# Kernel tuning notes

Measured on AMD Instinct MI355X. Metric: run time of the kernel, lower is better.

Reference implementation:

```python
import jax, jax.numpy as jnp
import numpy as np

EMBED_DIM = 128
N_HEADS = 8
TANH_CLIP = 10.0
NEG_INF = -1e9


def setup_inputs() -> dict:
    key = jax.random.key(0)
    k1, k2, k3, k4 = jax.random.split(key, 4)
    B, N, D = 512, 200, EMBED_DIM
    s = 1.0 / np.sqrt(D)
    return {
        "embeddings": jax.random.normal(k1, (B, N, D), dtype=jnp.float32),
        "W_node": jax.random.uniform(k2, (D, 3 * D), jnp.float32, -s, s),
        "W_fixed": jax.random.uniform(k3, (D, D), jnp.float32, -s, s),
        "W_step": jax.random.uniform(k4, (D, D), jnp.float32, -s, s),
    }


def _decode(embeddings, W_node, W_fixed, W_step):
    B, N, D = embeddings.shape
    H = N_HEADS
    dk = D // H

    # Precompute (once): glimpse K/V and logit K, plus fixed graph context.
    proj = embeddings @ W_node                      # [B,N,3D]
    gK, gV, lK = jnp.split(proj, 3, axis=-1)
    gK = gK.reshape(B, N, H, dk).transpose(0, 2, 1, 3)   # [B,H,N,dk]
    gV = gV.reshape(B, N, H, dk).transpose(0, 2, 1, 3)   # [B,H,N,dk]
    graph_emb = embeddings.mean(axis=1)             # [B,D]
    fixed_ctx = graph_emb @ W_fixed                 # [B,D]

    inv_sqrt_dk = 1.0 / jnp.sqrt(jnp.asarray(dk, embeddings.dtype))
    inv_sqrt_d = 1.0 / jnp.sqrt(jnp.asarray(D, embeddings.dtype))
    batch_idx = jnp.arange(B)

    def step(carry, _):
        visited, ctx_emb = carry                    # [B,N] bool, [B,D]
        q = fixed_ctx + ctx_emb @ W_step            # [B,D]
        qh = q.reshape(B, H, dk)                    # [B,H,dk]
        # glimpse multi-head attention (mask_inner=True)
        compat = jnp.einsum('bhd,bhnd->bhn', qh, gK) * inv_sqrt_dk
        compat = jnp.where(visited[:, None, :], NEG_INF, compat)
        attn = jax.nn.softmax(compat, axis=-1)
        glimpse = jnp.einsum('bhn,bhnd->bhd', attn, gV).reshape(B, D)
        # single-head logits with tanh clipping (mask_logits=True)
        logits = jnp.einsum('bd,bnd->bn', glimpse, lK) * inv_sqrt_d
        logits = TANH_CLIP * jnp.tanh(logits)
        logits = jnp.where(visited, NEG_INF, logits)
        log_p = jax.nn.log_softmax(logits, axis=-1)  # [B,N]
        sel = jnp.argmax(log_p, axis=-1)             # greedy [B]
        visited = visited.at[batch_idx, sel].set(True)
        ctx_emb = embeddings[batch_idx, sel]         # next step context
        return (visited, ctx_emb), (log_p, sel)

    init = (jnp.zeros((B, N), dtype=bool), graph_emb)
    _, (log_ps, sels) = jax.lax.scan(step, init, None, length=N)
    return log_ps.transpose(1, 0, 2), sels.transpose(1, 0)  # [B,T,N], [B,T]


def reference(embeddings, W_node, W_fixed, W_step):
    log_p, pi = _decode(embeddings, W_node, W_fixed, W_step)
    return log_p, pi
```

## Files before the change

### kernel.cpp

```cpp
#include <hip/hip_runtime.h>
#include <math.h>


#define Bsz 512
#define Nn  200
#define Dd  128
#define TANH_CLIP 10.0f
#define NEG_INF  -1e9f
#define LOG2E 1.4426950408889634f
#define LN2   0.6931471805599453f
#define QSCALE (0.25f * LOG2E)
#define LSCALE (0.08838834764831845f * 2.0f * LOG2E)

typedef float v2f __attribute__((ext_vector_type(2)));

__device__ __forceinline__ v2f pkfma(v2f a, v2f b, v2f c) {
    return __builtin_elementwise_fma(a, b, c);
}
__device__ __forceinline__ float fast_rcp(float x) { return __builtin_amdgcn_rcpf(x); }
__device__ __forceinline__ float fexp2(float x)    { return __builtin_amdgcn_exp2f(x); }
__device__ __forceinline__ float flog2(float x)    { return __builtin_amdgcn_logf(x); }
__device__ __forceinline__ float rdlane(float v, int l) {
    union { float f; int i; } u; u.f = v;
    u.i = __builtin_amdgcn_readlane(u.i, l);
    return u.f;
}

template <int CTRL, int RMASK, bool BC>
__device__ __forceinline__ float dppf(float x, float oldv) {
    int r = __builtin_amdgcn_update_dpp(__builtin_bit_cast(int, oldv),
                                        __builtin_bit_cast(int, x),
                                        CTRL, RMASK, 0xf, BC);
    return __builtin_bit_cast(float, r);
}
template <int CTRL, int RMASK, bool BC>
__device__ __forceinline__ int dppi(int x, int oldv) {
    return __builtin_amdgcn_update_dpp(oldv, x, CTRL, RMASK, 0xf, BC);
}
__device__ __forceinline__ float wave_sum63(float x) {
    x += dppf<0x111, 0xf, true >(x, 0.f);
    x += dppf<0x112, 0xf, true >(x, 0.f);
    x += dppf<0x114, 0xf, true >(x, 0.f);
    x += dppf<0x118, 0xf, true >(x, 0.f);
    x += dppf<0x142, 0xa, false>(x, 0.f);
    x += dppf<0x143, 0xc, false>(x, 0.f);
    return x;
}
__device__ __forceinline__ float wave_max63(float x) {
    x = fmaxf(x, dppf<0x111, 0xf, false>(x, -INFINITY));
    x = fmaxf(x, dppf<0x112, 0xf, false>(x, -INFINITY));
    x = fmaxf(x, dppf<0x114, 0xf, false>(x, -INFINITY));
    x = fmaxf(x, dppf<0x118, 0xf, false>(x, -INFINITY));
    x = fmaxf(x, dppf<0x142, 0xa, false>(x, -INFINITY));
    x = fmaxf(x, dppf<0x143, 0xc, false>(x, -INFINITY));
    return x;
}

__device__ __forceinline__ float dot16pk(const float4* g4, const float4* q4) {
    const v2f* g = (const v2f*)g4;
    const v2f* q = (const v2f*)q4;
    v2f a0 = g[0] * q[0];
    v2f a1 = g[1] * q[1];
    a0 = pkfma(g[2], q[2], a0);
    a1 = pkfma(g[3], q[3], a1);
    a0 = pkfma(g[4], q[4], a0);
    a1 = pkfma(g[5], q[5], a1);
    a0 = pkfma(g[6], q[6], a0);
    a1 = pkfma(g[7], q[7], a1);
    const v2f a = a0 + a1;
    return a.x + a.y;
}

__global__ __launch_bounds__(256, 3) void proj_kernel(
    const float* __restrict__ emb, const float* __restrict__ Wn,
    float* __restrict__ gk, float* __restrict__ gv, float* __restrict__ lk)
{
    const int bid = blockIdx.x;
    const int cg  = bid % 3;
    const int rowBase = (bid / 3) * 64;
    const int t  = threadIdx.x;
    const int c4 = t & 31;
    const int r8 = t >> 5;

    __shared__ __align__(16) float wn_s[64][128];
    __shared__ __align__(16) float e_s[64][68];

    float acc[8][4];
#pragma unroll
    for (int j = 0; j < 8; ++j)
#pragma unroll
        for (int m = 0; m < 4; ++m) acc[j][m] = 0.f;

    for (int kh = 0; kh < 2; ++kh) {
#pragma unroll
        for (int i = 0; i < 8; ++i) {
            const int idx = t + 256 * i;
            const int kr = idx >> 5, cc = (idx & 31) * 4;
            *(float4*)&wn_s[kr][cc] =
                *(const float4*)&Wn[(size_t)(kh * 64 + kr) * 384 + 128 * cg + cc];
        }
#pragma unroll
        for (int i = 0; i < 4; ++i) {
            const int idx = t + 256 * i;
            const int rr = idx >> 4, kk4 = (idx & 15) * 4;
            *(float4*)&e_s[rr][kk4] =
                *(const float4*)&emb[(size_t)(rowBase + rr) * Dd + kh * 64 + kk4];
        }
        __syncthreads();

#pragma unroll
        for (int k4 = 0; k4 < 16; ++k4) {
            float4 er[8];
#pragma unroll
            for (int j = 0; j < 8; ++j)
                er[j] = *(const float4*)&e_s[8 * r8 + j][4 * k4];
#pragma unroll
            for (int m = 0; m < 4; ++m) {
                const float4 wv = *(const float4*)&wn_s[4 * k4 + m][4 * c4];
#pragma unroll
                for (int j = 0; j < 8; ++j) {
                    const float ev = (m == 0) ? er[j].x : (m == 1) ? er[j].y
                                   : (m == 2) ? er[j].z : er[j].w;
                    acc[j][0] = fmaf(ev, wv.x, acc[j][0]);
                    acc[j][1] = fmaf(ev, wv.y, acc[j][1]);
                    acc[j][2] = fmaf(ev, wv.z, acc[j][2]);
                    acc[j][3] = fmaf(ev, wv.w, acc[j][3]);
                }
            }
        }
        __syncthreads();
    }

    float* out = (cg == 0) ? gk : (cg == 1) ? gv : lk;
    const float scl = (cg == 0) ? QSCALE : (cg == 2) ? LSCALE : 1.0f;
#pragma unroll
    for (int j = 0; j < 8; ++j) {
        float4 v;
        v.x = acc[j][0] * scl; v.y = acc[j][1] * scl;
        v.z = acc[j][2] * scl; v.w = acc[j][3] * scl;
        *(float4*)&out[(size_t)(rowBase + 8 * r8 + j) * Dd + 4 * c4] = v;
    }
}

__global__ __launch_bounds__(512, 2) void decode_kernel(
    const float* __restrict__ emb,
    const float* __restrict__ Wf,
    const float* __restrict__ Wsp,
    const float* __restrict__ gk, const float* __restrict__ gv,
    const float* __restrict__ lk,
    float* __restrict__ out_logp,
    float* __restrict__ out_pi)
{
    const int b    = blockIdx.x;
    const int t    = threadIdx.x;
    const int lane = t & 63;
    const int w    = t >> 6;
    const int g    = t >> 7;
    const int d    = t & 127;
    const int jq   = lane >> 2;
    const int kk   = lane & 3;

    __shared__ __align__(16) float qall_s[201 * Dd];
    __shared__ __align__(16) float wchunk_s[16][Dd];
    __shared__ __align__(16) float red[4][Dd];
    __shared__ __align__(16) float ctx0_s[Dd];
    __shared__ __align__(16) float fixedc_s[Dd];
    __shared__ __align__(16) float sm2[8][256];
    __shared__ __align__(16) float glimbc[8][16];
    __shared__             float smp[256 * 9];
    __shared__ __align__(16) float4 cand[8];

    const float* embB = emb + (size_t)b * Nn * Dd;
    const float* gkB  = gk  + (size_t)b * Nn * Dd;
    const float* gvB  = gv  + (size_t)b * Nn * Dd;
    const float* lkB  = lk  + (size_t)b * Nn * Dd;

    {
        const float4* e4  = (const float4*)embB;
        float4*       es4 = (float4*)qall_s;
#pragma unroll
        for (int it = 0; it < 12; ++it) es4[t + 512 * it] = e4[t + 512 * it];
        if (t < 256) es4[t + 6144] = e4[t + 6144];
    }
    __syncthreads();
    {
        float s = 0.f;
#pragma unroll
        for (int k = 0; k < 50; ++k) s += qall_s[(50 * g + k) * Dd + d];
        red[g][d] = s;
    }
    __syncthreads();
    if (t < 128) ctx0_s[t] = (red[0][t] + red[1][t] + red[2][t] + red[3][t]) * (1.0f / 200.0f);
    __syncthreads();
    {
        float s = 0.f;
#pragma unroll
        for (int j = 0; j < 32; ++j)
            s = fmaf(ctx0_s[32 * g + j], Wf[(32 * g + j) * Dd + d], s);
        red[g][d] = s;
    }
    __syncthreads();
    if (t < 128) {
        fixedc_s[t] = red[0][t] + red[1][t] + red[2][t] + red[3][t];
        qall_s[200 * Dd + t] = ctx0_s[t];
    }
    __syncthreads();

    float qr[52];
#pragma unroll
    for (int i = 0; i < 52; ++i) qr[i] = 0.f;
    for (int kc = 0; kc < 8; ++kc) {
        {
            const int kr = t >> 5, cc = (t & 31) * 4;
            *(float4*)&wchunk_s[kr][cc] =
                *(const float4*)&Wsp[(size_t)(16 * kc + kr) * Dd + cc];
        }
        __syncthreads();
#pragma unroll
        for (int i = 0; i < 52; ++i) {
            const int r = 52 * g + i;
            if (r < 201) {
#pragma unroll
                for (int j4 = 0; j4 < 4; ++j4) {
                    const float4 ev = *(const float4*)&qall_s[r * Dd + 16 * kc + 4 * j4];
                    qr[i] = fmaf(ev.x, wchunk_s[4 * j4 + 0][d], qr[i]);
                    qr[i] = fmaf(ev.y, wchunk_s[4 * j4 + 1][d], qr[i]);
                    qr[i] = fmaf(ev.z, wchunk_s[4 * j4 + 2][d], qr[i]);
                    qr[i] = fmaf(ev.w, wchunk_s[4 * j4 + 3][d], qr[i]);
                }
            }
        }
        __syncthreads();
    }
#pragma unroll
    for (int i = 0; i < 52; ++i) {
        const int r = 52 * g + i;
        if (r < 201) qall_s[r * Dd + d] = qr[i];
    }
    __syncthreads();

    float4 gk0[4], gk1[4], gk2[4], gk3[4];
    float4 lr[4][4];
    float  gva[52];
    float  cb[4];
    {
        const int n3 = (lane < 8) ? lane + 192 : 199;
        const float4* s0 = (const float4*)(gkB + (size_t)(lane      ) * Dd + 16 * w);
        const float4* s1 = (const float4*)(gkB + (size_t)(lane +  64) * Dd + 16 * w);
        const float4* s2 = (const float4*)(gkB + (size_t)(lane + 128) * Dd + 16 * w);
        const float4* s3 = (const float4*)(gkB + (size_t)n3 * Dd + 16 * w);
#pragma unroll
        for (int i = 0; i < 4; ++i) { gk0[i]=s0[i]; gk1[i]=s1[i]; gk2[i]=s2[i]; gk3[i]=s3[i]; }
        const float4* l0 = (const float4*)(lkB + (size_t)(lane      ) * Dd + 16 * w);
        const float4* l1 = (const float4*)(lkB + (size_t)(lane +  64) * Dd + 16 * w);
        const float4* l2 = (const float4*)(lkB + (size_t)(lane + 128) * Dd + 16 * w);
        const float4* l3 = (const float4*)(lkB + (size_t)n3 * Dd + 16 * w);
#pragma unroll
        for (int i = 0; i < 4; ++i) { lr[0][i]=l0[i]; lr[1][i]=l1[i]; lr[2][i]=l2[i]; lr[3][i]=l3[i]; }
    }
#pragma unroll
    for (int k = 0; k < 52; ++k) {
        int r = 52 * kk + k; r = r < 200 ? r : 199;
        gva[k] = gvB[(size_t)r * Dd + 16 * w + jq];
    }
    {
        float4 fcf[4];
        const float4* fcp = (const float4*)(fixedc_s + 16 * w);
#pragma unroll
        for (int i = 0; i < 4; ++i) fcf[i] = fcp[i];
        cb[0] = dot16pk(gk0, fcf);
        cb[1] = dot16pk(gk1, fcf);
        cb[2] = dot16pk(gk2, fcf);
        cb[3] = dot16pk(gk3, fcf);
    }

    const int nB = 32 * w + (lane >> 1);
    const int hB = lane & 1;

    unsigned int visA = 0;
    unsigned int visB = 0;
    int sel_prev = 200;

    for (int step = 0; step < Nn; ++step) {
        float4 qv[4];
        {
            const float4* qp = (const float4*)(qall_s + sel_prev * Dd + 16 * w);
            qv[0] = qp[0]; qv[1] = qp[1]; qv[2] = qp[2]; qv[3] = qp[3];
        }
        float p0, p1, p2, p3;
        {
            float x0 = dot16pk(gk0, qv) + cb[0];
            float x1 = dot16pk(gk1, qv) + cb[1];
            float x2 = dot16pk(gk2, qv) + cb[2];
            float x3 = dot16pk(gk3, qv) + cb[3];
            x0 = (visA & 1u) ? -1e30f : x0;
            x1 = (visA & 2u) ? -1e30f : x1;
            x2 = (visA & 4u) ? -1e30f : x2;
            x3 = (lane < 8 && !(visA & 8u)) ? x3 : -1e30f;
            p0 = fexp2(x0); p1 = fexp2(x1); p2 = fexp2(x2); p3 = fexp2(x3);
        }
        {
            float* prow = &sm2[w][0];
            prow[lane      ] = p0;
            prow[lane +  64] = p1;
            prow[lane + 128] = p2;
            prow[lane + 192] = p3;
        }
        float ps = (p0 + p1) + (p2 + p3);
#pragma unroll
        for (int off = 1; off < 64; off <<= 1) ps += __shfl_xor(ps, off);
        const float invps = fast_rcp(ps);

        {
            const float4* a4  = (const float4*)(&sm2[w][52 * kk]);
            float s0 = 0.f, s1 = 0.f, s2 = 0.f, s3 = 0.f;
#pragma unroll
            for (int k4 = 0; k4 < 13; ++k4) {
                const float4 av = a4[k4];
                s0 = fmaf(av.x, gva[4 * k4 + 0], s0);
                s1 = fmaf(av.y, gva[4 * k4 + 1], s1);
                s2 = fmaf(av.z, gva[4 * k4 + 2], s2);
                s3 = fmaf(av.w, gva[4 * k4 + 3], s3);
            }
            float gsum = (s0 + s1) + (s2 + s3);
            gsum += __shfl_xor(gsum, 1);
            gsum += __shfl_xor(gsum, 2);
            if (kk == 0) glimbc[w][jq] = gsum * invps;
        }
        float4 gw[4];
        {
            const float4* gbp = (const float4*)&glimbc[w][0];
            gw[0] = gbp[0]; gw[1] = gbp[1]; gw[2] = gbp[2]; gw[3] = gbp[3];
        }
        {
            const float a0 = dot16pk(lr[0], gw);
            const float a1 = dot16pk(lr[1], gw);
            const float a2 = dot16pk(lr[2], gw);
            const float a3 = dot16pk(lr[3], gw);
            smp[(lane      ) * 9 + w] = a0;
            smp[(lane +  64) * 9 + w] = a1;
            smp[(lane + 128) * 9 + w] = a2;
            if (lane < 8) smp[(lane + 192) * 9 + w] = a3;
        }
        __syncthreads();

        float lfin;
        {
            const int base = nB * 9 + 4 * hB;
            float s4 = (smp[base] + smp[base+1]) + (smp[base+2] + smp[base+3]);
            s4 += dppf<0xB1, 0xf, true>(s4, 0.f);
            const float u  = fexp2(s4);
            const float lv = TANH_CLIP - 2.0f * TANH_CLIP * fast_rcp(u + 1.0f);
            lfin = (nB >= Nn) ? -INFINITY : ((visB & 1u) ? NEG_INF : lv);
        }
        const float mx_s = rdlane(wave_max63(lfin), 63);
        const unsigned long long bal = __ballot(lfin == mx_s);
        const int sel_w = 32 * w + (__builtin_ctzll(bal) >> 1);
        float e = (hB == 0) ? fexp2((lfin - 10.f) * LOG2E) : 0.f;
        const float esum_w = wave_sum63(e);
        if (lane == 63) {
            float4 c;
            c.x = mx_s; c.y = __int_as_float(sel_w); c.z = esum_w; c.w = 0.f;
            cand[w] = c;
        }
        __syncthreads();

        int sel; float lse;
        {
            const float4 c = cand[lane & 7];
            float cv = c.x; int ci = __float_as_int(c.y); float ce = c.z;
#define CSTEP(CTRL) { \
            float ov = dppf<CTRL, 0xf, true>(cv, 0.f); \
            int   oi = dppi<CTRL, 0xf, true>(ci, 0);   \
            float oe = dppf<CTRL, 0xf, true>(ce, 0.f); \
            ce += oe; \
            if (ov > cv || (ov == cv && oi < ci)) { cv = ov; ci = oi; } }
            CSTEP(0xB1)
            CSTEP(0x4E)
            CSTEP(0x141)
#undef CSTEP
            sel = ci;
            lse = flog2(ce) * LN2 + 10.f;
        }

        if (hB == 0 && nB < Nn)
            out_logp[((size_t)b * Nn + step) * Nn + nB] = lfin - lse;
        if (t == 0) out_pi[(size_t)b * Nn + step] = (float)sel;

        visA |= (sel == lane)        ? 1u : 0u;
        visA |= (sel == lane + 64)   ? 2u : 0u;
        visA |= (sel == lane + 128)  ? 4u : 0u;
        visA |= (sel == lane + 192)  ? 8u : 0u;
        visB |= (sel == nB)          ? 1u : 0u;
        sel_prev = sel;
    }
}

extern "C" void kernel_launch(void* const* d_in, const int* in_sizes, int n_in,
                              void* d_out, int out_size, void* d_ws, size_t ws_size,
                              hipStream_t stream) {
    (void)in_sizes; (void)n_in; (void)out_size; (void)ws_size;
    const float* emb = (const float*)d_in[0];
    const float* Wn  = (const float*)d_in[1];
    const float* Wf  = (const float*)d_in[2];
    const float* Wsp = (const float*)d_in[3];

    const size_t BND = (size_t)Bsz * Nn * Dd;
    float* gk = (float*)d_ws;
    float* gv = gk + BND;
    float* lk = gv + BND;

    float* out_logp = (float*)d_out;
    float* out_pi   = out_logp + (size_t)Bsz * Nn * Nn;

    proj_kernel<<<(Bsz * Nn / 64) * 3, 256, 0, stream>>>(emb, Wn, gk, gv, lk);
    decode_kernel<<<Bsz, 512, 0, stream>>>(emb, Wf, Wsp, gk, gv, lk,
                                           out_logp, out_pi);
}
```

Before: 952.8 us.

## Move per-node query projection into proj kernel and drop decode shared-memory staging

New measurement: 1.016 ms. 6.7% more time.

```diff
diff --git a/kernel.cpp b/kernel.cpp
--- a/kernel.cpp
+++ b/kernel.cpp
@@ -73,17 +73,22 @@
 
 __global__ __launch_bounds__(256, 3) void proj_kernel(
     const float* __restrict__ emb, const float* __restrict__ Wn,
-    float* __restrict__ gk, float* __restrict__ gv, float* __restrict__ lk)
+    const float* __restrict__ Wsp,
+    float* __restrict__ gk, float* __restrict__ gv, float* __restrict__ lk,
+    float* __restrict__ qall)
 {
     const int bid = blockIdx.x;
-    const int cg  = bid % 3;
-    const int rowBase = (bid / 3) * 64;
+    const int cg  = bid & 3;
+    const int rowBase = (bid >> 2) * 64;
     const int t  = threadIdx.x;
     const int c4 = t & 31;
     const int r8 = t >> 5;
 
     __shared__ __align__(16) float wn_s[64][128];
     __shared__ __align__(16) float e_s[64][68];
+
+    const float* Wsrc  = (cg == 3) ? Wsp : (Wn + 128 * cg);
+    const int    wstr  = (cg == 3) ? 128 : 384;
 
     float acc[8][4];
 #pragma unroll
@@ -97,7 +102,7 @@
             const int idx = t + 256 * i;
             const int kr = idx >> 5, cc = (idx & 31) * 4;
             *(float4*)&wn_s[kr][cc] =
-                *(const float4*)&Wn[(size_t)(kh * 64 + kr) * 384 + 128 * cg + cc];
+                *(const float4*)&Wsrc[(size_t)(kh * 64 + kr) * wstr + cc];
         }
 #pragma unroll
         for (int i = 0; i < 4; ++i) {
@@ -131,7 +136,7 @@
         __syncthreads();
     }
 
-    float* out = (cg == 0) ? gk : (cg == 1) ? gv : lk;
+    float* out = (cg == 0) ? gk : (cg == 1) ? gv : (cg == 2) ? lk : qall;
     const float scl = (cg == 0) ? QSCALE : (cg == 2) ? LSCALE : 1.0f;
 #pragma unroll
     for (int j = 0; j < 8; ++j) {
@@ -142,12 +147,34 @@
     }
 }
 
+__global__ __launch_bounds__(128) void ctxprep_kernel(
+    const float* __restrict__ emb, const float* __restrict__ Wf,
+    const float* __restrict__ Wsp,
+    float* __restrict__ fixedc, float* __restrict__ q200)
+{
+    const int b = blockIdx.x, d = threadIdx.x;
+    __shared__ float c0[Dd];
+    const float* e = emb + (size_t)b * Nn * Dd;
+    float s = 0.f;
+    for (int n = 0; n < Nn; ++n) s += e[n * Dd + d];
+    s *= (1.0f / (float)Nn);
+    c0[d] = s;
+    __syncthreads();
+    float f = 0.f, q = 0.f;
+#pragma unroll 8
+    for (int k = 0; k < Dd; ++k) {
+        f = fmaf(c0[k], Wf[k * Dd + d], f);
+        q = fmaf(c0[k], Wsp[k * Dd + d], q);
+    }
+    fixedc[(size_t)b * Dd + d] = f;
+    q200[(size_t)b * Dd + d] = q;
+}
+
 __global__ __launch_bounds__(512, 2) void decode_kernel(
-    const float* __restrict__ emb,
-    const float* __restrict__ Wf,
-    const float* __restrict__ Wsp,
     const float* __restrict__ gk, const float* __restrict__ gv,
     const float* __restrict__ lk,
+    const float* __restrict__ qall, const float* __restrict__ q200,
+    const float* __restrict__ fixedc,
     float* __restrict__ out_logp,
     float* __restrict__ out_pi)
 {
@@ -155,89 +182,18 @@
     const int t    = threadIdx.x;
     const int lane = t & 63;
     const int w    = t >> 6;
-    const int g    = t >> 7;
-    const int d    = t & 127;
     const int jq   = lane >> 2;
     const int kk   = lane & 3;
 
-    __shared__ __align__(16) float qall_s[201 * Dd];
-    __shared__ __align__(16) float wchunk_s[16][Dd];
-    __shared__ __align__(16) float red[4][Dd];
-    __shared__ __align__(16) float ctx0_s[Dd];
-    __shared__ __align__(16) float fixedc_s[Dd];
     __shared__ __align__(16) float sm2[8][256];
     __shared__ __align__(16) float glimbc[8][16];
     __shared__             float smp[256 * 9];
     __shared__ __align__(16) float4 cand[8];
 
-    const float* embB = emb + (size_t)b * Nn * Dd;
     const float* gkB  = gk  + (size_t)b * Nn * Dd;
     const float* gvB  = gv  + (size_t)b * Nn * Dd;
     const float* lkB  = lk  + (size_t)b * Nn * Dd;
-
-    {
-        const float4* e4  = (const float4*)embB;
-        float4*       es4 = (float4*)qall_s;
-#pragma unroll
-        for (int it = 0; it < 12; ++it) es4[t + 512 * it] = e4[t + 512 * it];
-        if (t < 256) es4[t + 6144] = e4[t + 6144];
-    }
-    __syncthreads();
-    {
-        float s = 0.f;
-#pragma unroll
-        for (int k = 0; k < 50; ++k) s += qall_s[(50 * g + k) * Dd + d];
-        red[g][d] = s;
-    }
-    __syncthreads();
-    if (t < 128) ctx0_s[t] = (red[0][t] + red[1][t] + red[2][t] + red[3][t]) * (1.0f / 200.0f);
-    __syncthreads();
-    {
-        float s = 0.f;
-#pragma unroll
-        for (int j = 0; j < 32; ++j)
-            s = fmaf(ctx0_s[32 * g + j], Wf[(32 * g + j) * Dd + d], s);
-        red[g][d] = s;
-    }
-    __syncthreads();
-    if (t < 128) {
-        fixedc_s[t] = red[0][t] + red[1][t] + red[2][t] + red[3][t];
-        qall_s[200 * Dd + t] = ctx0_s[t];
-    }
-    __syncthreads();
-
-    float qr[52];
-#pragma unroll
-    for (int i = 0; i < 52; ++i) qr[i] = 0.f;
-    for (int kc = 0; kc < 8; ++kc) {
-        {
-            const int kr = t >> 5, cc = (t & 31) * 4;
-            *(float4*)&wchunk_s[kr][cc] =
-                *(const float4*)&Wsp[(size_t)(16 * kc + kr) * Dd + cc];
-        }
-        __syncthreads();
-#pragma unroll
-        for (int i = 0; i < 52; ++i) {
-            const int r = 52 * g + i;
-            if (r < 201) {
-#pragma unroll
-                for (int j4 = 0; j4 < 4; ++j4) {
-                    const float4 ev = *(const float4*)&qall_s[r * Dd + 16 * kc + 4 * j4];
-                    qr[i] = fmaf(ev.x, wchunk_s[4 * j4 + 0][d], qr[i]);
-                    qr[i] = fmaf(ev.y, wchunk_s[4 * j4 + 1][d], qr[i]);
-                    qr[i] = fmaf(ev.z, wchunk_s[4 * j4 + 2][d], qr[i]);
-                    qr[i] = fmaf(ev.w, wchunk_s[4 * j4 + 3][d], qr[i]);
-                }
-            }
-        }
-        __syncthreads();
-    }
-#pragma unroll
-    for (int i = 0; i < 52; ++i) {
-        const int r = 52 * g + i;
-        if (r < 201) qall_s[r * Dd + d] = qr[i];
-    }
-    __syncthreads();
+    const float* qaB  = qall + (size_t)b * Nn * Dd;
 
     float4 gk0[4], gk1[4], gk2[4], gk3[4];
     float4 lr[4][4];
@@ -265,7 +221,7 @@
     }
     {
         float4 fcf[4];
-        const float4* fcp = (const float4*)(fixedc_s + 16 * w);
+        const float4* fcp = (const float4*)(fixedc + (size_t)b * Dd + 16 * w);
 #pragma unroll
         for (int i = 0; i < 4; ++i) fcf[i] = fcp[i];
         cb[0] = dot16pk(gk0, fcf);
@@ -279,12 +235,14 @@
 
     unsigned int visA = 0;
     unsigned int visB = 0;
-    int sel_prev = 200;
+    int sel_prev = -1;
 
     for (int step = 0; step < Nn; ++step) {
         float4 qv[4];
         {
-            const float4* qp = (const float4*)(qall_s + sel_prev * Dd + 16 * w);
+            const float* rowp = (step == 0) ? (q200 + (size_t)b * Dd)
+                                            : (qaB + (size_t)sel_prev * Dd);
+            const float4* qp = (const float4*)(rowp + 16 * w);
             qv[0] = qp[0]; qv[1] = qp[1]; qv[2] = qp[2]; qv[3] = qp[3];
         }
         float p0, p1, p2, p3;
@@ -406,14 +364,19 @@
     const float* Wsp = (const float*)d_in[3];
 
     const size_t BND = (size_t)Bsz * Nn * Dd;
-    float* gk = (float*)d_ws;
-    float* gv = gk + BND;
-    float* lk = gv + BND;
+    float* gk     = (float*)d_ws;
+    float* gv     = gk + BND;
+    float* lk     = gv + BND;
+    float* qall   = lk + BND;
+    float* q200   = qall + BND;
+    float* fixedc = q200 + (size_t)Bsz * Dd;
 
     float* out_logp = (float*)d_out;
     float* out_pi   = out_logp + (size_t)Bsz * Nn * Nn;
 
-    proj_kernel<<<(Bsz * Nn / 64) * 3, 256, 0, stream>>>(emb, Wn, gk, gv, lk);
-    decode_kernel<<<Bsz, 512, 0, stream>>>(emb, Wf, Wsp, gk, gv, lk,
+    proj_kernel<<<(Bsz * Nn / 64) * 4, 256, 0, stream>>>(emb, Wn, Wsp,
+                                                         gk, gv, lk, qall);
+    ctxprep_kernel<<<Bsz, 128, 0, stream>>>(emb, Wf, Wsp, fixedc, q200);
+    decode_kernel<<<Bsz, 512, 0, stream>>>(gk, gv, lk, qall, q200, fixedc,
                                            out_logp, out_pi);
 }
```
